# Performance work log

Measured on AMD Instinct MI355X. Metric: run time of the kernel, lower is better.

The kernel has to match this reference:

```python
import jax, jax.numpy as jnp
import numpy as np

E = 8      # num_experts
K = 2      # top-k
DIM = 1024
DFF = 2048  # fused gate+up width; intermediate = DFF // 2 == DIM


def setup_inputs() -> dict:
    key = jax.random.key(0)
    ks = jax.random.split(key, 5)
    B, S = 4, 2048
    x = jax.random.normal(ks[0], (B, S, DIM), dtype=jnp.float32)
    Wg = jax.random.normal(ks[1], (E, DIM), dtype=jnp.float32) * 0.02
    bg = jax.random.normal(ks[2], (E,), dtype=jnp.float32) * 0.02
    w1 = jax.random.normal(ks[3], (E, DFF, DIM), dtype=jnp.float32) * 0.02
    w2 = jax.random.normal(ks[4], (E, DIM, DFF // 2), dtype=jnp.float32) * 0.02
    return {"x": x, "Wg": Wg, "bg": bg, "w1": w1, "w2": w2}


def _moe(x, Wg, bg, w1, w2):
    B, S, D = x.shape
    t = x.reshape(-1, D)                      # [T, D] tokens
    logits = t @ Wg.T + bg                    # [T, E]
    probs = jax.nn.softmax(logits, axis=-1)
    topw, topi = jax.lax.top_k(probs, K)      # [T, K]
    topw = topw / jnp.sum(topw, axis=-1, keepdims=True)  # renormalize=True
    # per-token combine weight for each expert (0 if not selected): [T, E]
    combine = jnp.sum(jax.nn.one_hot(topi, E, dtype=t.dtype) * topw[..., None], axis=1)

    def body(acc, packed):
        w1e, w2e, ce = packed                 # [DFF, D], [D, DFF//2], [T]
        h = t @ w1e.T                         # [T, DFF]
        gate, up = jnp.split(h, 2, axis=-1)   # silu_and_mul (SwiGLU)
        a = jax.nn.silu(gate) * up            # [T, DFF//2]
        o = a @ w2e.T                         # [T, D]
        return acc + ce[:, None] * o, None

    out, _ = jax.lax.scan(body, jnp.zeros_like(t), (w1, w2, combine.T))
    return out.reshape(B, S, D)


def reference(x, Wg, bg, w1, w2):
    return _moe(x, Wg, bg, w1, w2)
```

## Files before the change

### kernel.cpp

```cpp
#include <hip/hip_runtime.h>
#include <hip/hip_bf16.h>
#include <cstdint>

#define T_TOKENS 8192
#define DIM 1024
#define NEXP 8
#define DFFH 1024
#define ROWCAP 17408
#define NCHUNK 16
#define MAXMTA 12
#define MAXMTB 24
#define NGATEB 128
#define NCASTB 1920

typedef __attribute__((ext_vector_type(8))) short bf16x8;
typedef __attribute__((ext_vector_type(16))) float f32x16;

__device__ __forceinline__ ushort f2bf(float f) {
  uint32_t u = __float_as_uint(f);
  uint32_t r = (u + 0x7fffu + ((u >> 16) & 1u)) >> 16;
  return (ushort)r;
}
__device__ __forceinline__ float bf2f(ushort u) {
  return __uint_as_float(((uint32_t)u) << 16);
}

__device__ __forceinline__ void async16(const void* g, const void* l) {
  __builtin_amdgcn_global_load_lds(
      (const __attribute__((address_space(1))) void*)(uintptr_t)g,
      (__attribute__((address_space(3))) void*)(uintptr_t)l, 16, 0, 0);
}

__global__ __launch_bounds__(256) void gatecast_kernel(
    const float4* __restrict__ x4, const float4* __restrict__ Wg4,
    const float* __restrict__ bg, const float4* __restrict__ w1,
    const float4* __restrict__ w2, int* __restrict__ top2e,
    float2* __restrict__ top2w, ushort* __restrict__ xb,
    ushort* __restrict__ w1b, ushort* __restrict__ w2b,
    int* __restrict__ blkcnt ) {
  __shared__ float4 wgl[NEXP * 256];
  __shared__ int lcnt[NEXP];
  const int tid = threadIdx.x;

  if (blockIdx.x >= NGATEB) {
    const int NW1 = NEXP * 2048 * DIM / 4;
    const int NW2 = NEXP * DIM * DFFH / 4;
    const int total = NW1 + NW2;
    const int cb = blockIdx.x - NGATEB;
    for (int i = cb * 256 + tid; i < total; i += NCASTB * 256) {
      float4 v; ushort* dst;
      if (i < NW1) { v = w1[i]; dst = w1b + (size_t)i * 4; }
      else { int j = i - NW1; v = w2[j]; dst = w2b + (size_t)j * 4; }
      ushort4 o4;
      o4.x = f2bf(v.x); o4.y = f2bf(v.y); o4.z = f2bf(v.z); o4.w = f2bf(v.w);
      *(ushort4*)dst = o4;
    }
    return;
  }

  for (int i = tid; i < NEXP * 256; i += 256) wgl[i] = Wg4[i];
  if (tid < NEXP) lcnt[tid] = 0;
  __syncthreads();
  const int wave = tid >> 6, lane = tid & 63;
  const float bgsel = bg[lane & 7];
  const int t0 = (blockIdx.x * 4 + wave) * 16;
  for (int tt = 0; tt < 16; ++tt) {
    const int t = t0 + tt;
    const float4* xr = x4 + (size_t)t * 256;
    ushort4* xw = (ushort4*)(xb + (size_t)t * DIM);
    float acc[NEXP];
#pragma unroll
    for (int e = 0; e < NEXP; ++e) acc[e] = 0.f;
#pragma unroll
    for (int j = 0; j < 4; ++j) {
      float4 xv = xr[lane + j * 64];
      ushort4 o4;
      o4.x = f2bf(xv.x); o4.y = f2bf(xv.y); o4.z = f2bf(xv.z); o4.w = f2bf(xv.w);
      xw[lane + j * 64] = o4;
#pragma unroll
      for (int e = 0; e < NEXP; ++e) {
        float4 wv = wgl[e * 256 + lane + j * 64];
        acc[e] += xv.x * wv.x + xv.y * wv.y + xv.z * wv.z + xv.w * wv.w;
      }
    }
#pragma unroll
    for (int e = 0; e < NEXP; ++e) {
      float v = acc[e];
      v += __shfl_xor(v, 1); v += __shfl_xor(v, 2); v += __shfl_xor(v, 4);
      acc[e] = v;
    }
    float v = acc[0];
#pragma unroll
    for (int e = 1; e < NEXP; ++e) v = ((lane & 7) == e) ? acc[e] : v;
    v += __shfl_xor(v, 8); v += __shfl_xor(v, 16); v += __shfl_xor(v, 32);
    v += bgsel;
    float m1 = v;
    m1 = fmaxf(m1, __shfl_xor(m1, 1));
    m1 = fmaxf(m1, __shfl_xor(m1, 2));
    m1 = fmaxf(m1, __shfl_xor(m1, 4));
    unsigned long long mk = __ballot(v == m1);
    int bi = (int)(__ffsll(mk) - 1) & 7;
    float v2 = (((lane & 7) == bi) ? -1e30f : v);
    float m2 = v2;
    m2 = fmaxf(m2, __shfl_xor(m2, 1));
    m2 = fmaxf(m2, __shfl_xor(m2, 2));
    m2 = fmaxf(m2, __shfl_xor(m2, 4));
    mk = __ballot(v2 == m2);
    int si = (int)(__ffsll(mk) - 1) & 7;
    if (lane == 0) {
      float w0 = 1.f / (1.f + __expf(m2 - m1));
      top2e[t] = bi | (si << 8);
      top2w[t] = make_float2(w0, 1.f - w0);
      atomicAdd(&lcnt[bi], 1);
      atomicAdd(&lcnt[si], 1);
    }
  }
  __syncthreads();
  if (tid < NEXP) blkcnt[blockIdx.x * NEXP + tid] = lcnt[tid];
}

__global__ __launch_bounds__(512) void scatter_kernel(
    const int* __restrict__ top2e, const float2* __restrict__ top2w,
    const int* __restrict__ blkcnt, int* __restrict__ rows_token,
    float* __restrict__ rows_weight, int2* __restrict__ tok2row,
    int* __restrict__ cnt, int* __restrict__ off) {
  __shared__ int s_all[NGATEB * NEXP];
  __shared__ int s_tot[NEXP], s_pre[NEXP];
  __shared__ int s_base[NEXP];
  __shared__ int lcnt[NEXP];
  const int tid = threadIdx.x;
  const int b = blockIdx.x;
  s_all[tid] = blkcnt[tid];
  s_all[512 + tid] = blkcnt[512 + tid];
  if (tid < NEXP) lcnt[tid] = 0;
  __syncthreads();
  if (tid < NEXP) {
    int tot = 0, pre = 0;
    const int cutoff = b * (NGATEB / NCHUNK);
#pragma unroll 1
    for (int k = 0; k < NGATEB; ++k) {
      int v = s_all[k * NEXP + tid];
      tot += v;
      if (k < cutoff) pre += v;
    }
    s_tot[tid] = tot; s_pre[tid] = pre;
  }
  __syncthreads();
  if (tid == 0) {
    int o = 0;
#pragma unroll
    for (int e = 0; e < NEXP; ++e) {
      s_base[e] = o + s_pre[e];
      if (b == 0) { cnt[e] = s_tot[e]; off[e] = o; }
      o += (s_tot[e] + 127) & ~127;
    }
    if (b == 0) off[NEXP] = o;
  }
  __syncthreads();
  const int t = b * 512 + tid;
  int pk = top2e[t];
  float2 w = top2w[t];
  int e0 = pk & 255, e1 = (pk >> 8) & 255;
  int p0 = atomicAdd(&lcnt[e0], 1);
  int p1 = atomicAdd(&lcnt[e1], 1);
  int r0 = s_base[e0] + p0;
  int r1 = s_base[e1] + p1;
  rows_token[r0] = t; rows_weight[r0] = w.x;
  rows_token[r1] = t; rows_weight[r1] = w.y;
  tok2row[t] = make_int2(r0, r1);
}

__global__ __launch_bounds__(512, 2) void mlpA_kernel(
    const ushort* __restrict__ xb, const ushort* __restrict__ w1b,
    const int* __restrict__ rows_token, const int* __restrict__ cnt,
    const int* __restrict__ off, ushort* __restrict__ abuf) {
  const int bid = blockIdx.x;
  const int e = bid & 7;
  const int pos = bid >> 3;
  const int mt = pos >> 3, nt = pos & 7;
  const int count = cnt[e];
  if (mt * 256 >= count) return;
  const int base = off[e];
  const int padcnt = off[e + 1] - base;

  __shared__ ushort As[2][256 * 64];
  __shared__ ushort Bg[2][128 * 64];
  __shared__ ushort Bu[2][128 * 64];

  const int tid = threadIdx.x;
  const int wave = tid >> 6, lane = tid & 63;
  const int wm = wave >> 2, wn = wave & 3;
  const int cg = tid & 7;
  const int r7 = (tid >> 3) & 7;
  const int cgs = (cg ^ r7) * 8;

  const ushort* gA[4];
#pragma unroll
  for (int i = 0; i < 4; ++i) {
    int row = i * 64 + (tid >> 3);
    int r = mt * 256 + row;
    int tok = (r < count) ? rows_token[base + r] : 0;
    gA[i] = xb + ((size_t)tok * DIM + cgs);
  }
  const ushort* gG[2];
  const ushort* gU[2];
#pragma unroll
  for (int i = 0; i < 2; ++i) {
    int row = i * 64 + (tid >> 3);
    gG[i] = w1b + ((size_t)(e * 2048 + nt * 128 + row) * DIM + cgs);
    gU[i] = w1b + ((size_t)(e * 2048 + 1024 + nt * 128 + row) * DIM + cgs);
  }

#define STAGE_A1(b_, k0_)                                           \
  {                                                                 \
    _Pragma("unroll")                                               \
    for (int i = 0; i < 4; ++i)                                     \
      async16(gA[i] + (k0_), &As[b_][(i * 512 + tid) * 8]);         \
    _Pragma("unroll")                                               \
    for (int i = 0; i < 2; ++i) {                                   \
      async16(gG[i] + (k0_), &Bg[b_][(i * 512 + tid) * 8]);         \
      async16(gU[i] + (k0_), &Bu[b_][(i * 512 + tid) * 8]);         \
    }                                                               \
  }

  const f32x16 zz = {0,0,0,0,0,0,0,0,0,0,0,0,0,0,0,0};
  f32x16 ag[4] = {zz, zz, zz, zz};
  f32x16 au[4] = {zz, zz, zz, zz};

  const int xr = (lane & 7) << 3;
  const int la31 = lane & 31;
  const int kbase = (lane >> 5) * 8;

#define COMPA(b_)                                                               \
  {                                                                             \
    _Pragma("unroll")                                                           \
    for (int kk = 0; kk < 4; ++kk) {                                            \
      const int ko = (kk * 16 + kbase) ^ xr;                                    \
      bf16x8 bg_ = *(const bf16x8*)&Bg[b_][(wn * 32 + la31) * 64 + ko];         \
      bf16x8 bu_ = *(const bf16x8*)&Bu[b_][(wn * 32 + la31) * 64 + ko];         \
      bf16x8 a0 = *(const bf16x8*)&As[b_][(wm * 128 + la31) * 64 + ko];         \
      bf16x8 a1 = *(const bf16x8*)&As[b_][(wm * 128 + 32 + la31) * 64 + ko];    \
      bf16x8 a2 = *(const bf16x8*)&As[b_][(wm * 128 + 64 + la31) * 64 + ko];    \
      bf16x8 a3 = *(const bf16x8*)&As[b_][(wm * 128 + 96 + la31) * 64 + ko];    \
      ag[0] = __builtin_amdgcn_mfma_f32_32x32x16_bf16(a0, bg_, ag[0], 0, 0, 0); \
      ag[1] = __builtin_amdgcn_mfma_f32_32x32x16_bf16(a1, bg_, ag[1], 0, 0, 0); \
      ag[2] = __builtin_amdgcn_mfma_f32_32x32x16_bf16(a2, bg_, ag[2], 0, 0, 0); \
      ag[3] = __builtin_amdgcn_mfma_f32_32x32x16_bf16(a3, bg_, ag[3], 0, 0, 0); \
      au[0] = __builtin_amdgcn_mfma_f32_32x32x16_bf16(a0, bu_, au[0], 0, 0, 0); \
      au[1] = __builtin_amdgcn_mfma_f32_32x32x16_bf16(a1, bu_, au[1], 0, 0, 0); \
      au[2] = __builtin_amdgcn_mfma_f32_32x32x16_bf16(a2, bu_, au[2], 0, 0, 0); \
      au[3] = __builtin_amdgcn_mfma_f32_32x32x16_bf16(a3, bu_, au[3], 0, 0, 0); \
    }                                                                           \
  }

  STAGE_A1(0, 0);
  __syncthreads();
#pragma unroll
  for (int it = 0; it < 8; ++it) {
    STAGE_A1(1, it * 128 + 64);
    COMPA(0);
    __syncthreads();
    if (it < 7) STAGE_A1(0, it * 128 + 128);
    COMPA(1);
    __syncthreads();
  }

  const int colg = nt * 128 + wn * 32 + la31;
  const int rlo = 4 * (lane >> 5);
#pragma unroll
  for (int m = 0; m < 4; ++m) {
#pragma unroll
    for (int r = 0; r < 16; ++r) {
      int rr = (r & 3) + 8 * (r >> 2) + rlo;
      int row = mt * 256 + wm * 128 + m * 32 + rr;
      if (row < padcnt) {
        float g = ag[m][r], u = au[m][r];
        float a = (g / (1.f + __expf(-g))) * u;
        abuf[(size_t)(base + row) * DFFH + colg] = f2bf(a);
      }
    }
  }
#undef STAGE_A1
#undef COMPA
}

__global__ __launch_bounds__(256) void mlpB_kernel(
    const ushort* __restrict__ abuf, const ushort* __restrict__ w2b,
    const float* __restrict__ rows_weight, const int* __restrict__ cnt,
    const int* __restrict__ off, ushort* __restrict__ obuf) {
  const int bid = blockIdx.x;
  const int e = bid & 7;
  const int pos = bid >> 3;
  const int mt = pos >> 3, nt = pos & 7;
  const int count = cnt[e];
  if (mt * 128 >= count) return;
  const int base = off[e];

  __shared__ ushort As[2][128 * 64];
  __shared__ ushort Bs[2][128 * 64];

  const int tid = threadIdx.x;
  const int wave = tid >> 6, lane = tid & 63;
  const int wm = wave >> 1, wn = wave & 1;
  const int cg = tid & 7;
  const int r7w = (tid >> 3) & 7;
  const int cgs = (cg ^ r7w) * 8;

  const ushort* gA[4];
#pragma unroll
  for (int i = 0; i < 4; ++i) {
    int row = i * 32 + (tid >> 3);
    gA[i] = abuf + ((size_t)(base + mt * 128 + row) * DFFH + cgs);
  }
  const ushort* gB[4];
#pragma unroll
  for (int i = 0; i < 4; ++i) {
    int row = i * 32 + (tid >> 3);
    gB[i] = w2b + ((size_t)(e * 1024 + nt * 128 + row) * DFFH + cgs);
  }

#define STAGE_B1(b_, k0_)                                           \
  {                                                                 \
    _Pragma("unroll")                                               \
    for (int i = 0; i < 4; ++i) {                                   \
      async16(gA[i] + (k0_), &As[b_][(i * 256 + wave * 64) * 8]);   \
      async16(gB[i] + (k0_), &Bs[b_][(i * 256 + wave * 64) * 8]);   \
    }                                                               \
  }

  f32x16 acc00 = {0,0,0,0,0,0,0,0,0,0,0,0,0,0,0,0};
  f32x16 acc01 = acc00, acc10 = acc00, acc11 = acc00;

  const int xr = (lane & 7) << 3;
  const int la31 = lane & 31;
  const int kbase = (lane >> 5) * 8;

#define COMPB(b_)                                                              \
  {                                                                            \
    _Pragma("unroll")                                                          \
    for (int kk = 0; kk < 4; ++kk) {                                           \
      const int ko = (kk * 16 + kbase) ^ xr;                                   \
      bf16x8 a0 = *(const bf16x8*)&As[b_][(wm * 64 + la31) * 64 + ko];         \
      bf16x8 a1 = *(const bf16x8*)&As[b_][(wm * 64 + 32 + la31) * 64 + ko];    \
      bf16x8 b0 = *(const bf16x8*)&Bs[b_][(wn * 64 + la31) * 64 + ko];         \
      bf16x8 b1 = *(const bf16x8*)&Bs[b_][(wn * 64 + 32 + la31) * 64 + ko];    \
      acc00 = __builtin_amdgcn_mfma_f32_32x32x16_bf16(a0, b0, acc00, 0, 0, 0); \
      acc01 = __builtin_amdgcn_mfma_f32_32x32x16_bf16(a0, b1, acc01, 0, 0, 0); \
      acc10 = __builtin_amdgcn_mfma_f32_32x32x16_bf16(a1, b0, acc10, 0, 0, 0); \
      acc11 = __builtin_amdgcn_mfma_f32_32x32x16_bf16(a1, b1, acc11, 0, 0, 0); \
    }                                                                          \
  }

  STAGE_B1(0, 0);
  __syncthreads();
#pragma unroll
  for (int it = 0; it < 8; ++it) {
    STAGE_B1(1, it * 128 + 64);
    COMPB(0);
    __syncthreads();
    if (it < 7) STAGE_B1(0, it * 128 + 128);
    COMPB(1);
    __syncthreads();
  }

  const int rlo = 4 * (lane >> 5);
  const int colb = nt * 128 + wn * 64 + la31;
#pragma unroll
  for (int s = 0; s < 2; ++s) {
    const f32x16 c0 = s ? acc10 : acc00;
    const f32x16 c1 = s ? acc11 : acc01;
#pragma unroll
    for (int r = 0; r < 16; ++r) {
      int rr = (r & 3) + 8 * (r >> 2) + rlo;
      int lrow = mt * 128 + wm * 64 + s * 32 + rr;
      if (lrow < count) {
        float wgt = rows_weight[base + lrow];
        obuf[(size_t)(base + lrow) * DIM + colb] = f2bf(wgt * c0[r]);
        obuf[(size_t)(base + lrow) * DIM + colb + 32] = f2bf(wgt * c1[r]);
      }
    }
  }
#undef STAGE_B1
#undef COMPB
}

__global__ __launch_bounds__(256) void combine_kernel(
    const ushort* __restrict__ obuf, const int2* __restrict__ tok2row,
    float* __restrict__ out) {
  const int t = blockIdx.x;
  int2 rr = tok2row[t];
  const ushort4* p0 = (const ushort4*)(obuf + (size_t)rr.x * DIM);
  const ushort4* p1 = (const ushort4*)(obuf + (size_t)rr.y * DIM);
  float4* po = (float4*)(out + (size_t)t * DIM);
  const int c = threadIdx.x;
  ushort4 a = p0[c], b = p1[c];
  float4 o;
  o.x = bf2f(a.x) + bf2f(b.x);
  o.y = bf2f(a.y) + bf2f(b.y);
  o.z = bf2f(a.z) + bf2f(b.z);
  o.w = bf2f(a.w) + bf2f(b.w);
  po[c] = o;
}

extern "C" void kernel_launch(void* const* d_in, const int* in_sizes, int n_in,
                              void* d_out, int out_size, void* d_ws, size_t ws_size,
                              hipStream_t stream) {
  const float* x = (const float*)d_in[0];
  const float* Wg = (const float*)d_in[1];
  const float* bg = (const float*)d_in[2];
  const float* w1 = (const float*)d_in[3];
  const float* w2 = (const float*)d_in[4];
  float* out = (float*)d_out;

  char* ws = (char*)d_ws;
  ushort* xb = (ushort*)ws;
  ushort* w1b = xb + (size_t)T_TOKENS * DIM;
  ushort* w2b = w1b + (size_t)NEXP * 2048 * DIM;
  ushort* abuf = w2b + (size_t)NEXP * DIM * DFFH;
  char* p = (char*)(abuf + (size_t)ROWCAP * DFFH);
  int* top2e = (int*)p;            p += T_TOKENS * 4;
  float2* top2w = (float2*)p;      p += T_TOKENS * 8;
  int* rows_token = (int*)p;       p += ROWCAP * 4;
  float* rows_weight = (float*)p;  p += ROWCAP * 4;
  int2* tok2row = (int2*)p;        p += T_TOKENS * 8;
  int* cnt = (int*)p;              p += 32;
  int* off = (int*)p;              p += 64;
  int* blkcnt = (int*)p;           p += NGATEB * NEXP * 4;
  ushort* obuf = xb;

  gatecast_kernel<<<NGATEB + NCASTB, 256, 0, stream>>>(
      (const float4*)x, (const float4*)Wg, bg, (const float4*)w1,
      (const float4*)w2, top2e, top2w, xb, w1b, w2b, blkcnt);
  scatter_kernel<<<NCHUNK, 512, 0, stream>>>(top2e, top2w, blkcnt, rows_token,
                                             rows_weight, tok2row, cnt, off);
  mlpA_kernel<<<8 * MAXMTA * 8, 512, 0, stream>>>(xb, w1b, rows_token, cnt, off, abuf);
  mlpB_kernel<<<8 * MAXMTB * 8, 256, 0, stream>>>(abuf, w2b, rows_weight, cnt, off, obuf);
  combine_kernel<<<T_TOKENS, 256, 0, stream>>>(obuf, tok2row, out);
}
```

Measured before the change: 251.3 us.

## Restructure mlpA main loop into fine-grained staged pipeline with 16x16x32 MFMA

The mlpA gate/up GEMM loop is rewritten so each K-tile is split into four sub-stages. Loads of the next tile's B-gate, A-half0, B-up and A-half1 are interleaved with reads from the current tile and MFMA work, using explicit vmcnt/lgkmcnt waits, raw s_barrier, sched_barrier and setprio. It switches from 32x32x16 to 16x16x32 bf16 MFMA with a new per-wave tile mapping and epilogue indexing. The aim is to hide global-to-LDS latency and cut full __syncthreads stalls. In exchange it adds hand-tuned waitcnt logic that is fragile and could be racy if the counts are wrong.

Result: faster. 239.8 us (-4.6%).

```diff
diff --git a/kernel.cpp b/kernel.cpp
--- a/kernel.cpp
+++ b/kernel.cpp
@@ -14,7 +14,13 @@
 #define NCASTB 1920
 
 typedef __attribute__((ext_vector_type(8))) short bf16x8;
+typedef __attribute__((ext_vector_type(4))) float f32x4;
 typedef __attribute__((ext_vector_type(16))) float f32x16;
+
+#define VMWAIT(n) asm volatile("s_waitcnt vmcnt(" #n ")" ::: "memory")
+#define LGKM0     asm volatile("s_waitcnt lgkmcnt(0)" ::: "memory")
+#define SBAR      __builtin_amdgcn_s_barrier()
+#define SCHEDB    __builtin_amdgcn_sched_barrier(0)
 
 __device__ __forceinline__ ushort f2bf(float f) {
   uint32_t u = __float_as_uint(f);
@@ -184,21 +190,17 @@
   const int padcnt = off[e + 1] - base;
 
   __shared__ ushort As[2][256 * 64];
-  __shared__ ushort Bg[2][128 * 64];
-  __shared__ ushort Bu[2][128 * 64];
+  __shared__ ushort Bs[2][2][128 * 64];
 
   const int tid = threadIdx.x;
   const int wave = tid >> 6, lane = tid & 63;
   const int wm = wave >> 2, wn = wave & 3;
-  const int cg = tid & 7;
-  const int r7 = (tid >> 3) & 7;
-  const int cgs = (cg ^ r7) * 8;
+  const int cgs = ((tid & 7) ^ ((tid >> 3) & 7)) * 8;
 
   const ushort* gA[4];
 #pragma unroll
   for (int i = 0; i < 4; ++i) {
-    int row = i * 64 + (tid >> 3);
-    int r = mt * 256 + row;
+    int r = mt * 256 + i * 64 + (tid >> 3);
     int tok = (r < count) ? rows_token[base + r] : 0;
     gA[i] = xb + ((size_t)tok * DIM + cgs);
   }
@@ -211,77 +213,103 @@
     gU[i] = w1b + ((size_t)(e * 2048 + 1024 + nt * 128 + row) * DIM + cgs);
   }
 
-#define STAGE_A1(b_, k0_)                                           \
-  {                                                                 \
-    _Pragma("unroll")                                               \
-    for (int i = 0; i < 4; ++i)                                     \
-      async16(gA[i] + (k0_), &As[b_][(i * 512 + tid) * 8]);         \
-    _Pragma("unroll")                                               \
-    for (int i = 0; i < 2; ++i) {                                   \
-      async16(gG[i] + (k0_), &Bg[b_][(i * 512 + tid) * 8]);         \
-      async16(gU[i] + (k0_), &Bu[b_][(i * 512 + tid) * 8]);         \
-    }                                                               \
-  }
-
-  const f32x16 zz = {0,0,0,0,0,0,0,0,0,0,0,0,0,0,0,0};
-  f32x16 ag[4] = {zz, zz, zz, zz};
-  f32x16 au[4] = {zz, zz, zz, zz};
+#define STG_BG(b_, k_) { async16(gG[0]+(k_), &Bs[b_][0][tid*8]);     async16(gG[1]+(k_), &Bs[b_][0][(512+tid)*8]); }
+#define STG_A0(b_, k_) { async16(gA[0]+(k_), &As[b_][tid*8]);        async16(gA[1]+(k_), &As[b_][(512+tid)*8]); }
+#define STG_BU(b_, k_) { async16(gU[0]+(k_), &Bs[b_][1][tid*8]);     async16(gU[1]+(k_), &Bs[b_][1][(512+tid)*8]); }
+#define STG_A1(b_, k_) { async16(gA[2]+(k_), &As[b_][(1024+tid)*8]); async16(gA[3]+(k_), &As[b_][(1536+tid)*8]); }
+
+  const f32x4 z4 = {0.f, 0.f, 0.f, 0.f};
+  f32x4 aG[8][2], aU[8][2];
+#pragma unroll
+  for (int m = 0; m < 8; ++m)
+#pragma unroll
+    for (int n = 0; n < 2; ++n) { aG[m][n] = z4; aU[m][n] = z4; }
 
   const int xr = (lane & 7) << 3;
-  const int la31 = lane & 31;
-  const int kbase = (lane >> 5) * 8;
-
-#define COMPA(b_)                                                               \
-  {                                                                             \
-    _Pragma("unroll")                                                           \
-    for (int kk = 0; kk < 4; ++kk) {                                            \
-      const int ko = (kk * 16 + kbase) ^ xr;                                    \
-      bf16x8 bg_ = *(const bf16x8*)&Bg[b_][(wn * 32 + la31) * 64 + ko];         \
-      bf16x8 bu_ = *(const bf16x8*)&Bu[b_][(wn * 32 + la31) * 64 + ko];         \
-      bf16x8 a0 = *(const bf16x8*)&As[b_][(wm * 128 + la31) * 64 + ko];         \
-      bf16x8 a1 = *(const bf16x8*)&As[b_][(wm * 128 + 32 + la31) * 64 + ko];    \
-      bf16x8 a2 = *(const bf16x8*)&As[b_][(wm * 128 + 64 + la31) * 64 + ko];    \
-      bf16x8 a3 = *(const bf16x8*)&As[b_][(wm * 128 + 96 + la31) * 64 + ko];    \
-      ag[0] = __builtin_amdgcn_mfma_f32_32x32x16_bf16(a0, bg_, ag[0], 0, 0, 0); \
-      ag[1] = __builtin_amdgcn_mfma_f32_32x32x16_bf16(a1, bg_, ag[1], 0, 0, 0); \
-      ag[2] = __builtin_amdgcn_mfma_f32_32x32x16_bf16(a2, bg_, ag[2], 0, 0, 0); \
-      ag[3] = __builtin_amdgcn_mfma_f32_32x32x16_bf16(a3, bg_, ag[3], 0, 0, 0); \
-      au[0] = __builtin_amdgcn_mfma_f32_32x32x16_bf16(a0, bu_, au[0], 0, 0, 0); \
-      au[1] = __builtin_amdgcn_mfma_f32_32x32x16_bf16(a1, bu_, au[1], 0, 0, 0); \
-      au[2] = __builtin_amdgcn_mfma_f32_32x32x16_bf16(a2, bu_, au[2], 0, 0, 0); \
-      au[3] = __builtin_amdgcn_mfma_f32_32x32x16_bf16(a3, bu_, au[3], 0, 0, 0); \
-    }                                                                           \
-  }
-
-  STAGE_A1(0, 0);
-  __syncthreads();
-#pragma unroll
-  for (int it = 0; it < 8; ++it) {
-    STAGE_A1(1, it * 128 + 64);
-    COMPA(0);
-    __syncthreads();
-    if (it < 7) STAGE_A1(0, it * 128 + 128);
-    COMPA(1);
-    __syncthreads();
-  }
-
-  const int colg = nt * 128 + wn * 32 + la31;
-  const int rlo = 4 * (lane >> 5);
-#pragma unroll
-  for (int m = 0; m < 4; ++m) {
-#pragma unroll
-    for (int r = 0; r < 16; ++r) {
-      int rr = (r & 3) + 8 * (r >> 2) + rlo;
-      int row = mt * 256 + wm * 128 + m * 32 + rr;
-      if (row < padcnt) {
-        float g = ag[m][r], u = au[m][r];
-        float a = (g / (1.f + __expf(-g))) * u;
-        abuf[(size_t)(base + row) * DFFH + colg] = f2bf(a);
+  const int la15 = lane & 15;
+  const int kb = (lane >> 4) * 8;
+
+  bf16x8 fa[4][2], fbg[2][2], fbu[2][2];
+
+#define KO(kk_) (((kk_) * 32 + kb) ^ xr)
+#define RD_A(b_, h_)                                                              \
+  { _Pragma("unroll") for (int i = 0; i < 4; ++i)                                 \
+    _Pragma("unroll") for (int kk = 0; kk < 2; ++kk)                              \
+      fa[i][kk] = *(const bf16x8*)&As[b_][((h_)*128 + wm*64 + i*16 + la15)*64 + KO(kk)]; }
+#define RD_BG(b_)                                                                 \
+  { _Pragma("unroll") for (int n = 0; n < 2; ++n)                                 \
+    _Pragma("unroll") for (int kk = 0; kk < 2; ++kk)                              \
+      fbg[n][kk] = *(const bf16x8*)&Bs[b_][0][(wn*32 + n*16 + la15)*64 + KO(kk)]; }
+#define RD_BU(b_)                                                                 \
+  { _Pragma("unroll") for (int n = 0; n < 2; ++n)                                 \
+    _Pragma("unroll") for (int kk = 0; kk < 2; ++kk)                              \
+      fbu[n][kk] = *(const bf16x8*)&Bs[b_][1][(wn*32 + n*16 + la15)*64 + KO(kk)]; }
+#define MMH(acc_, h_, fb_)                                                        \
+  { __builtin_amdgcn_s_setprio(1);                                               \
+    _Pragma("unroll") for (int kk = 0; kk < 2; ++kk)                              \
+    _Pragma("unroll") for (int i = 0; i < 4; ++i)                                 \
+    _Pragma("unroll") for (int n = 0; n < 2; ++n)                                 \
+      acc_[(h_)*4 + i][n] = __builtin_amdgcn_mfma_f32_16x16x32_bf16(              \
+          fa[i][kk], fb_[n][kk], acc_[(h_)*4 + i][n], 0, 0, 0);                   \
+    __builtin_amdgcn_s_setprio(0); }
+
+#define TILE(bc_, bn_, k_, SG_, VA_, VB_, VC_)                                    \
+  { VMWAIT(VA_); SBAR; SCHEDB;                     \
+    RD_BG(bc_); RD_A(bc_, 0);                                                     \
+    if (SG_) STG_BG(bn_, k_);                                                     \
+    LGKM0; SCHEDB;                                                                \
+    MMH(aG, 0, fbg);                                                              \
+    VMWAIT(VB_); SBAR; SCHEDB;                                   \
+    RD_BU(bc_);                                                                   \
+    if (SG_) STG_A0(bn_, k_);                                                     \
+    LGKM0; SCHEDB;                                                                \
+    MMH(aU, 0, fbu);                                                              \
+    VMWAIT(VC_); SBAR; SCHEDB;                                   \
+    RD_A(bc_, 1);                                                                 \
+    if (SG_) STG_BU(bn_, k_);                                                     \
+    LGKM0; SCHEDB;                                                                \
+    MMH(aG, 1, fbg);                                                              \
+    if (SG_) STG_A1(bn_, k_);                                                     \
+    MMH(aU, 1, fbu); }
+
+  STG_BG(0, 0); STG_A0(0, 0); STG_BU(0, 0); STG_A1(0, 0);
+
+#pragma unroll 1
+  for (int tt = 0; tt < 7; ++tt) {
+    const int k1 = (2 * tt + 1) * 64, k2 = (2 * tt + 2) * 64;
+    TILE(0, 1, k1, 1, 4, 4, 4);
+    TILE(1, 0, k2, 1, 4, 4, 4);
+  }
+  TILE(0, 1, 960, 1, 4, 4, 4);
+  TILE(1, 1, 0, 0, 4, 2, 0);
+
+  const int colg = nt * 128 + wn * 32 + la15;
+  const int rlo = (lane >> 4) * 4;
+#pragma unroll
+  for (int m = 0; m < 8; ++m) {
+#pragma unroll
+    for (int n = 0; n < 2; ++n) {
+#pragma unroll
+      for (int r = 0; r < 4; ++r) {
+        int row = mt * 256 + (m >> 2) * 128 + wm * 64 + (m & 3) * 16 + rlo + r;
+        if (row < padcnt) {
+          float g = aG[m][n][r], u = aU[m][n][r];
+          float a = (g / (1.f + __expf(-g))) * u;
+          abuf[(size_t)(base + row) * DFFH + colg + n * 16] = f2bf(a);
+        }
       }
     }
   }
-#undef STAGE_A1
-#undef COMPA
+#undef STG_BG
+#undef STG_A0
+#undef STG_BU
+#undef STG_A1
+#undef RD_A
+#undef RD_BG
+#undef RD_BU
+#undef MMH
+#undef TILE
+#undef KO
 }
 
 __global__ __launch_bounds__(256) void mlpB_kernel(
```
